# Performance work log

Hardware: AMD Instinct MI355X
Metric: run time of the kernel (lower is better)

Reference implementation:

```python
import jax, jax.numpy as jnp
import numpy as np

B, T, C = 2, 4096, 512
P, PS, CS, MB, FD = 64, 16, 5, 128, 128


def setup_inputs() -> dict:
    key = jax.random.key(0)
    ks = jax.random.split(key, 9)
    y = jax.random.normal(ks[0], (B, T, C), jnp.float32)
    # per-timestep random patch indices into the sequence axis, sorted per patch
    patches = jnp.sort(jax.random.randint(ks[1], (T, P, PS), 0, T), axis=-1).astype(jnp.int32)
    patches_proj = jax.random.randint(ks[2], (T, P), 0, T).astype(jnp.int32)
    W_BASE = jax.random.normal(ks[3], (P, PS, CS), jnp.float32) * 0.05
    W_BIAS = jax.random.normal(ks[4], (P,), jnp.float32) * 0.05
    W_proj2 = jax.random.normal(ks[5], (C, MB), jnp.float32) * (1.0 / np.sqrt(C).astype(np.float32))
    W_proj_comp = jax.random.normal(ks[6], (C, CS), jnp.float32) * (1.0 / np.sqrt(C).astype(np.float32))
    W_presoftmax1 = jax.random.normal(ks[7], (P, P), jnp.float32) * (1.0 / np.sqrt(P).astype(np.float32))
    W_FINAL = jax.random.normal(ks[8], (MB, FD), jnp.float32) * (1.0 / np.sqrt(MB).astype(np.float32))
    return {
        'y': y,
        'W_BASE': W_BASE,
        'W_BIAS': W_BIAS,
        'W_proj2': W_proj2,
        'W_proj_comp': W_proj_comp,
        'W_presoftmax1': W_presoftmax1,
        'W_FINAL': W_FINAL,
        'patches': patches,
        'patches_proj': patches_proj,
    }


def reference(y, W_BASE, W_BIAS, W_proj2, W_proj_comp, W_presoftmax1, W_FINAL, patches, patches_proj):
    # value branch: project then gather one sequence element per (t, patch)
    bm = jnp.einsum('btc,cm->btm', y, W_proj2)          # [B,T,MB]
    mbg = bm[:, patches_proj, :]                        # [B,T,P,MB]  (MBMB)
    # score branch: compress, gather PS elements per (t, patch), weighted reduce
    yc = jnp.einsum('btc,ck->btk', y, W_proj_comp)      # [B,T,CS]
    g = yc[:, patches, :]                               # [B,T,P,PS,CS]
    res = jnp.einsum('btpsc,psc->btp', g, W_BASE) + W_BIAS   # [B,T,P]
    mix = jnp.einsum('btp,pq->btq', res, W_presoftmax1)      # [B,T,P] (no softmax in source)
    out = jnp.einsum('btp,btpm->btm', mix, mbg)              # [B,T,MB]
    return jnp.einsum('btm,mf->btf', out, W_FINAL)           # [B,T,FD]
```

## Files before the change

### kernel.cpp

```cpp
#include <hip/hip_runtime.h>
#include <hip/hip_bf16.h>

#define B_ 2
#define T_ 4096
#define C_ 512
#define P_ 64
#define PS_ 16
#define CS_ 5
#define MB_ 128
#define FD_ 128

__device__ __forceinline__ float bf_lo(unsigned u) {
  return __uint_as_float(u << 16);
}
__device__ __forceinline__ float bf_hi(unsigned u) {
  return __uint_as_float(u & 0xffff0000u);
}
__device__ __forceinline__ float rdlane_f(float v, int p) {
  return __uint_as_float((unsigned)__builtin_amdgcn_readlane((int)__float_as_uint(v), p));
}

__global__ __launch_bounds__(256) void k_prep(const float* __restrict__ y,
                                              const float* __restrict__ Wc,
                                              __hip_bfloat16* __restrict__ ycp) {
  const int lane = threadIdx.x & 63;
  const int wid  = threadIdx.x >> 6;
  float wc[40];
  {
    const float4* src = (const float4*)(Wc + lane * 40);
    #pragma unroll
    for (int j = 0; j < 10; j++) {
      float4 v = src[j];
      wc[j*4+0] = v.x; wc[j*4+1] = v.y; wc[j*4+2] = v.z; wc[j*4+3] = v.w;
    }
  }
  const int row_base = (blockIdx.x * 4 + wid) * 4;
  #pragma unroll 1
  for (int r = 0; r < 4; r++) {
    const int row = row_base + r;
    const float4* yr = (const float4*)(y + (size_t)row * C_ + lane * 8);
    float4 a = yr[0], b4 = yr[1];
    float s0 = 0.f, s1 = 0.f, s2 = 0.f, s3 = 0.f, s4 = 0.f;
    float e[8] = {a.x, a.y, a.z, a.w, b4.x, b4.y, b4.z, b4.w};
    #pragma unroll
    for (int j = 0; j < 8; j++) {
      s0 = fmaf(e[j], wc[j*5+0], s0);
      s1 = fmaf(e[j], wc[j*5+1], s1);
      s2 = fmaf(e[j], wc[j*5+2], s2);
      s3 = fmaf(e[j], wc[j*5+3], s3);
      s4 = fmaf(e[j], wc[j*5+4], s4);
    }
    #pragma unroll
    for (int off = 1; off < 64; off <<= 1) {
      s0 += __shfl_xor(s0, off); s1 += __shfl_xor(s1, off);
      s2 += __shfl_xor(s2, off); s3 += __shfl_xor(s3, off);
      s4 += __shfl_xor(s4, off);
    }
    float myv = (lane == 0) ? s0 : (lane == 1) ? s1 : (lane == 2) ? s2
              : (lane == 3) ? s3 : (lane == 4) ? s4 : 0.f;
    if (lane < 8) ycp[(size_t)row * 8 + lane] = __float2bfloat16(myv);
  }
}

__global__ __launch_bounds__(512) void k_bm(const float* __restrict__ y,
                                            const float* __restrict__ W,
                                            __hip_bfloat16* __restrict__ bmb) {
  __shared__ __align__(16) float ys[32 * 64];
  const int tid = threadIdx.x;
  const int row0 = blockIdx.x * 32;
  const int tn = tid & 127;
  const int tm = tid >> 7;
  float acc[8];
  #pragma unroll
  for (int r = 0; r < 8; r++) acc[r] = 0.f;
  for (int cc = 0; cc < C_; cc += 64) {
    __syncthreads();
    {
      int r = tid >> 4, c4 = tid & 15;
      *(float4*)&ys[r*64 + c4*4] =
          *(const float4*)&y[(size_t)(row0 + r) * C_ + cc + c4*4];
    }
    __syncthreads();
    #pragma unroll
    for (int c4 = 0; c4 < 16; c4++) {
      const int c = cc + c4*4;
      const float w0 = W[(size_t)(c+0)*MB_ + tn], w1 = W[(size_t)(c+1)*MB_ + tn],
                  w2 = W[(size_t)(c+2)*MB_ + tn], w3 = W[(size_t)(c+3)*MB_ + tn];
      #pragma unroll
      for (int r = 0; r < 8; r++) {
        float4 v = *(float4*)&ys[(tm*8 + r)*64 + c4*4];
        acc[r] = fmaf(v.x, w0, fmaf(v.y, w1, fmaf(v.z, w2, fmaf(v.w, w3, acc[r]))));
      }
    }
  }
  #pragma unroll
  for (int r = 0; r < 8; r++)
    bmb[(size_t)(row0 + tm*8 + r) * MB_ + tn] = __float2bfloat16(acc[r]);
}

__global__ __launch_bounds__(256, 2) void k_mid(
    const __hip_bfloat16* __restrict__ ycp,
    const __hip_bfloat16* __restrict__ bmb,
    const float* __restrict__ WB,
    const float* __restrict__ Wbias,
    const float* __restrict__ Wps1,
    const int* __restrict__ patches,
    const int* __restrict__ pproj,
    float* __restrict__ obm)
{
  const int lane = threadIdx.x & 63;
  const int wid  = threadIdx.x >> 6;
  const int gw   = blockIdx.x * 4 + wid;

  float wb[80];
  {
    const float4* src = (const float4*)(WB + lane * 80);
    #pragma unroll
    for (int j = 0; j < 20; j++) {
      float4 v = src[j];
      wb[j*4+0] = v.x; wb[j*4+1] = v.y; wb[j*4+2] = v.z; wb[j*4+3] = v.w;
    }
  }
  const float bias = Wbias[lane];
  float wcol[64];
  #pragma unroll
  for (int p = 0; p < 64; p++) wcol[p] = Wps1[p * 64 + lane];

  #pragma unroll 1
  for (int tt = 0; tt < 2; tt++) {
    const int t = gw * 2 + tt;
    int idx[16];
    {
      const int4* psrc = (const int4*)(patches + (size_t)t * P_ * PS_ + lane * PS_);
      #pragma unroll
      for (int j = 0; j < 4; j++) {
        int4 v = psrc[j];
        idx[j*4+0] = v.x; idx[j*4+1] = v.y; idx[j*4+2] = v.z; idx[j*4+3] = v.w;
      }
    }
    const int pp = pproj[(size_t)t * P_ + lane];

    #pragma unroll 1
    for (int b = 0; b < B_; b++) {
      const __hip_bfloat16* yb = ycp + (size_t)b * T_ * 8;
      float sum = bias;
      #pragma unroll
      for (int s = 0; s < 16; s++) {
        uint4 g = *(const uint4*)(yb + (size_t)idx[s] * 8);
        sum = fmaf(bf_lo(g.x), wb[s*5+0], sum);
        sum = fmaf(bf_hi(g.x), wb[s*5+1], sum);
        sum = fmaf(bf_lo(g.y), wb[s*5+2], sum);
        sum = fmaf(bf_hi(g.y), wb[s*5+3], sum);
        sum = fmaf(bf_lo(g.z), wb[s*5+4], sum);
      }
      float mix = 0.f;
      #pragma unroll
      for (int p = 0; p < 64; p++)
        mix = fmaf(rdlane_f(sum, p), wcol[p], mix);
      const __hip_bfloat16* bb = bmb + (size_t)b * T_ * MB_;
      float ox = 0.f, oy = 0.f;
      #pragma unroll
      for (int p = 0; p < 64; p++) {
        const float mp = rdlane_f(mix, p);
        const int row = __builtin_amdgcn_readlane(pp, p);
        unsigned v = *(const unsigned*)(bb + (size_t)row * MB_ + lane * 2);
        ox = fmaf(bf_lo(v), mp, ox);
        oy = fmaf(bf_hi(v), mp, oy);
      }
      float2 o2 = make_float2(ox, oy);
      *(float2*)(obm + ((size_t)b * T_ + t) * MB_ + lane * 2) = o2;
    }
  }
}

__global__ __launch_bounds__(512) void k_final(const float* __restrict__ obm,
                                               const float* __restrict__ WF,
                                               float* __restrict__ outp) {
  __shared__ __align__(16) float os[32 * MB_];
  const int tid = threadIdx.x;
  const int row0 = blockIdx.x * 32;
  for (int j = tid; j < 32 * MB_ / 4; j += 512)
    ((float4*)os)[j] = ((const float4*)(obm + (size_t)row0 * MB_))[j];
  __syncthreads();
  const int tn = tid & 127, tm = tid >> 7;
  float acc[8];
  #pragma unroll
  for (int r = 0; r < 8; r++) acc[r] = 0.f;
  #pragma unroll
  for (int m4 = 0; m4 < MB_ / 4; m4++) {
    const int m = m4 * 4;
    const float w0 = WF[(size_t)(m+0)*FD_ + tn], w1 = WF[(size_t)(m+1)*FD_ + tn],
                w2 = WF[(size_t)(m+2)*FD_ + tn], w3 = WF[(size_t)(m+3)*FD_ + tn];
    #pragma unroll
    for (int r = 0; r < 8; r++) {
      float4 v = *(float4*)&os[(tm*8 + r)*MB_ + m];
      acc[r] = fmaf(v.x, w0, fmaf(v.y, w1, fmaf(v.z, w2, fmaf(v.w, w3, acc[r]))));
    }
  }
  #pragma unroll
  for (int r = 0; r < 8; r++)
    outp[(size_t)(row0 + tm*8 + r) * FD_ + tn] = acc[r];
}

extern "C" void kernel_launch(void* const* d_in, const int* in_sizes, int n_in,
                              void* d_out, int out_size, void* d_ws, size_t ws_size,
                              hipStream_t stream) {
  const float* y     = (const float*)d_in[0];
  const float* WB    = (const float*)d_in[1];
  const float* Wbias = (const float*)d_in[2];
  const float* Wp2   = (const float*)d_in[3];
  const float* Wpc   = (const float*)d_in[4];
  const float* Wps1  = (const float*)d_in[5];
  const float* WF    = (const float*)d_in[6];
  const int* patches = (const int*)d_in[7];
  const int* pproj   = (const int*)d_in[8];
  float* out = (float*)d_out;

  char* ws = (char*)d_ws;
  float* obm          = (float*)(ws);
  __hip_bfloat16* bmb = (__hip_bfloat16*)(ws + 4194304);
  __hip_bfloat16* ycp = (__hip_bfloat16*)(ws + 6291456);

  k_prep <<<dim3(512), dim3(256), 0, stream>>>(y, Wpc, ycp);
  k_bm   <<<dim3(256), dim3(512), 0, stream>>>(y, Wp2, bmb);
  k_mid  <<<dim3(512), dim3(256), 0, stream>>>(ycp, bmb, WB, Wbias, Wps1,
                                               patches, pproj, obm);
  k_final<<<dim3(256), dim3(512), 0, stream>>>(obm, WF, out);
}
```

Baseline: 184.0 us.

## Replace scalar FP32 projection GEMMs with bf16 MFMA GEMM kernel

Converts y and the two projection weights to bf16 (weights transposed) and replaces the scalar FMA k_bm and k_final GEMMs with a shared templated MFMA 16x16x32 bf16 GEMM that uses a swizzled LDS layout. k_mid now writes its intermediate in bf16, halving that traffic, and k_prep also emits bf16 y. The goal is to move the dense projections onto matrix cores. In exchange it adds an extra weight-conversion launch, writes a bf16 copy of y, and loses precision from bf16 inputs to the final GEMM.

Result: faster. 151.1 us (-17.9%).

```diff
diff --git a/kernel.cpp b/kernel.cpp
--- a/kernel.cpp
+++ b/kernel.cpp
@@ -10,19 +10,28 @@
 #define MB_ 128
 #define FD_ 128
 
-__device__ __forceinline__ float bf_lo(unsigned u) {
+using f32x4 = __attribute__((ext_vector_type(4))) float;
+using s16x8 = __attribute__((ext_vector_type(8))) short;
+
+static __device__ __forceinline__ float bf_lo(unsigned u) {
   return __uint_as_float(u << 16);
 }
-__device__ __forceinline__ float bf_hi(unsigned u) {
+static __device__ __forceinline__ float bf_hi(unsigned u) {
   return __uint_as_float(u & 0xffff0000u);
 }
-__device__ __forceinline__ float rdlane_f(float v, int p) {
+static __device__ __forceinline__ float rdlane_f(float v, int p) {
   return __uint_as_float((unsigned)__builtin_amdgcn_readlane((int)__float_as_uint(v), p));
 }
-
-__global__ __launch_bounds__(256) void k_prep(const float* __restrict__ y,
-                                              const float* __restrict__ Wc,
-                                              __hip_bfloat16* __restrict__ ycp) {
+static __device__ __forceinline__ ushort bf16u(float f) {
+  unsigned x = __float_as_uint(f);
+  unsigned r = (x + 0x7fffu + ((x >> 16) & 1u)) >> 16;
+  return (ushort)r;
+}
+
+__global__ __launch_bounds__(256) void k_cvt(const float* __restrict__ y,
+                                             const float* __restrict__ Wc,
+                                             ushort* __restrict__ ybf,
+                                             ushort* __restrict__ ycp) {
   const int lane = threadIdx.x & 63;
   const int wid  = threadIdx.x >> 6;
   float wc[40];
@@ -34,14 +43,18 @@
       wc[j*4+0] = v.x; wc[j*4+1] = v.y; wc[j*4+2] = v.z; wc[j*4+3] = v.w;
     }
   }
-  const int row_base = (blockIdx.x * 4 + wid) * 4;
-  #pragma unroll 1
-  for (int r = 0; r < 4; r++) {
+  const int row_base = (blockIdx.x * 4 + wid) * 8;
+  #pragma unroll 2
+  for (int r = 0; r < 8; r++) {
     const int row = row_base + r;
     const float4* yr = (const float4*)(y + (size_t)row * C_ + lane * 8);
     float4 a = yr[0], b4 = yr[1];
+    float e[8] = {a.x, a.y, a.z, a.w, b4.x, b4.y, b4.z, b4.w};
+    union { ushort us[8]; uint4 q; } pk;
+    #pragma unroll
+    for (int j = 0; j < 8; j++) pk.us[j] = bf16u(e[j]);
+    *(uint4*)(ybf + (size_t)row * C_ + lane * 8) = pk.q;
     float s0 = 0.f, s1 = 0.f, s2 = 0.f, s3 = 0.f, s4 = 0.f;
-    float e[8] = {a.x, a.y, a.z, a.w, b4.x, b4.y, b4.z, b4.w};
     #pragma unroll
     for (int j = 0; j < 8; j++) {
       s0 = fmaf(e[j], wc[j*5+0], s0);
@@ -58,55 +71,115 @@
     }
     float myv = (lane == 0) ? s0 : (lane == 1) ? s1 : (lane == 2) ? s2
               : (lane == 3) ? s3 : (lane == 4) ? s4 : 0.f;
-    if (lane < 8) ycp[(size_t)row * 8 + lane] = __float2bfloat16(myv);
-  }
-}
-
-__global__ __launch_bounds__(512) void k_bm(const float* __restrict__ y,
-                                            const float* __restrict__ W,
-                                            __hip_bfloat16* __restrict__ bmb) {
-  __shared__ __align__(16) float ys[32 * 64];
-  const int tid = threadIdx.x;
-  const int row0 = blockIdx.x * 32;
-  const int tn = tid & 127;
-  const int tm = tid >> 7;
-  float acc[8];
+    if (lane < 8) ycp[(size_t)row * 8 + lane] = bf16u(myv);
+  }
+}
+
+__global__ __launch_bounds__(256) void k_cvtW(const float* __restrict__ Wp2,
+                                              const float* __restrict__ WF,
+                                              ushort* __restrict__ Wp2T,
+                                              ushort* __restrict__ WFT) {
+  const int id = blockIdx.x * 256 + threadIdx.x;
+  if (id < C_ * MB_) {
+    const int c = id >> 7, m = id & 127;
+    Wp2T[(size_t)m * C_ + c] = bf16u(Wp2[id]);
+  }
+  const int id2 = id - C_ * MB_;
+  if (id2 >= 0 && id2 < MB_ * FD_) {
+    const int m = id2 >> 7, f = id2 & 127;
+    WFT[(size_t)f * MB_ + m] = bf16u(WF[id2]);
+  }
+}
+
+template<int KTOT, bool OUTBF>
+__global__ __launch_bounds__(256) void k_gemm(const ushort* __restrict__ A,
+                                              const ushort* __restrict__ Bt,
+                                              void* __restrict__ Cout) {
+  __shared__ __align__(16) char smem[(64 + 128) * 128];
+  const int tid  = threadIdx.x;
+  const int lane = tid & 63;
+  const int wid  = tid >> 6;
+  const int wm = wid >> 1, wn = wid & 1;
+  const int rowA0 = blockIdx.x * 64;
+
+  f32x4 acc[2][4];
   #pragma unroll
-  for (int r = 0; r < 8; r++) acc[r] = 0.f;
-  for (int cc = 0; cc < C_; cc += 64) {
+  for (int m = 0; m < 2; m++)
+    #pragma unroll
+    for (int n = 0; n < 4; n++) acc[m][n] = (f32x4){0.f, 0.f, 0.f, 0.f};
+
+  for (int step = 0; step < KTOT / 64; step++) {
+    const int kc = step * 64;
+    uint4 ra[2], rb[4];
+    #pragma unroll
+    for (int i = 0; i < 2; i++) {
+      const int slot = tid + i * 256, r = slot >> 3, sl = slot & 7;
+      ra[i] = *(const uint4*)(A + (size_t)(rowA0 + r) * KTOT + kc + sl * 8);
+    }
+    #pragma unroll
+    for (int i = 0; i < 4; i++) {
+      const int slot = tid + i * 256, r = slot >> 3, sl = slot & 7;
+      rb[i] = *(const uint4*)(Bt + (size_t)r * KTOT + kc + sl * 8);
+    }
     __syncthreads();
-    {
-      int r = tid >> 4, c4 = tid & 15;
-      *(float4*)&ys[r*64 + c4*4] =
-          *(const float4*)&y[(size_t)(row0 + r) * C_ + cc + c4*4];
+    #pragma unroll
+    for (int i = 0; i < 2; i++) {
+      const int slot = tid + i * 256, r = slot >> 3, sl = slot & 7;
+      *(uint4*)(smem + r * 128 + ((sl * 16) ^ ((r & 7) << 4))) = ra[i];
+    }
+    #pragma unroll
+    for (int i = 0; i < 4; i++) {
+      const int slot = tid + i * 256, r = slot >> 3, sl = slot & 7;
+      *(uint4*)(smem + 8192 + r * 128 + ((sl * 16) ^ ((r & 7) << 4))) = rb[i];
     }
     __syncthreads();
     #pragma unroll
-    for (int c4 = 0; c4 < 16; c4++) {
-      const int c = cc + c4*4;
-      const float w0 = W[(size_t)(c+0)*MB_ + tn], w1 = W[(size_t)(c+1)*MB_ + tn],
-                  w2 = W[(size_t)(c+2)*MB_ + tn], w3 = W[(size_t)(c+3)*MB_ + tn];
-      #pragma unroll
-      for (int r = 0; r < 8; r++) {
-        float4 v = *(float4*)&ys[(tm*8 + r)*64 + c4*4];
-        acc[r] = fmaf(v.x, w0, fmaf(v.y, w1, fmaf(v.z, w2, fmaf(v.w, w3, acc[r]))));
-      }
+    for (int kk = 0; kk < 2; kk++) {
+      const int cb = kk * 64 + (lane >> 4) * 16;
+      s16x8 a[2], b[4];
+      #pragma unroll
+      for (int m = 0; m < 2; m++) {
+        const int r = wm * 32 + m * 16 + (lane & 15);
+        a[m] = *(const s16x8*)(smem + r * 128 + (cb ^ ((r & 7) << 4)));
+      }
+      #pragma unroll
+      for (int n = 0; n < 4; n++) {
+        const int rn = wn * 64 + n * 16 + (lane & 15);
+        b[n] = *(const s16x8*)(smem + 8192 + rn * 128 + (cb ^ ((rn & 7) << 4)));
+      }
+      #pragma unroll
+      for (int m = 0; m < 2; m++)
+        #pragma unroll
+        for (int n = 0; n < 4; n++)
+          acc[m][n] = __builtin_amdgcn_mfma_f32_16x16x32_bf16(a[m], b[n], acc[m][n], 0, 0, 0);
     }
   }
   #pragma unroll
-  for (int r = 0; r < 8; r++)
-    bmb[(size_t)(row0 + tm*8 + r) * MB_ + tn] = __float2bfloat16(acc[r]);
+  for (int m = 0; m < 2; m++) {
+    #pragma unroll
+    for (int n = 0; n < 4; n++) {
+      #pragma unroll
+      for (int reg = 0; reg < 4; reg++) {
+        const int grow = rowA0 + wm * 32 + m * 16 + (lane >> 4) * 4 + reg;
+        const int gcol = wn * 64 + n * 16 + (lane & 15);
+        if (OUTBF)
+          ((ushort*)Cout)[(size_t)grow * 128 + gcol] = bf16u(acc[m][n][reg]);
+        else
+          ((float*)Cout)[(size_t)grow * 128 + gcol] = acc[m][n][reg];
+      }
+    }
+  }
 }
 
 __global__ __launch_bounds__(256, 2) void k_mid(
-    const __hip_bfloat16* __restrict__ ycp,
-    const __hip_bfloat16* __restrict__ bmb,
+    const ushort* __restrict__ ycp,
+    const ushort* __restrict__ bmb,
     const float* __restrict__ WB,
     const float* __restrict__ Wbias,
     const float* __restrict__ Wps1,
     const int* __restrict__ patches,
     const int* __restrict__ pproj,
-    float* __restrict__ obm)
+    ushort* __restrict__ obmb)
 {
   const int lane = threadIdx.x & 63;
   const int wid  = threadIdx.x >> 6;
@@ -142,7 +215,7 @@
 
     #pragma unroll 1
     for (int b = 0; b < B_; b++) {
-      const __hip_bfloat16* yb = ycp + (size_t)b * T_ * 8;
+      const ushort* yb = ycp + (size_t)b * T_ * 8;
       float sum = bias;
       #pragma unroll
       for (int s = 0; s < 16; s++) {
@@ -157,7 +230,7 @@
       #pragma unroll
       for (int p = 0; p < 64; p++)
         mix = fmaf(rdlane_f(sum, p), wcol[p], mix);
-      const __hip_bfloat16* bb = bmb + (size_t)b * T_ * MB_;
+      const ushort* bb = bmb + (size_t)b * T_ * MB_;
       float ox = 0.f, oy = 0.f;
       #pragma unroll
       for (int p = 0; p < 64; p++) {
@@ -167,39 +240,10 @@
         ox = fmaf(bf_lo(v), mp, ox);
         oy = fmaf(bf_hi(v), mp, oy);
       }
-      float2 o2 = make_float2(ox, oy);
-      *(float2*)(obm + ((size_t)b * T_ + t) * MB_ + lane * 2) = o2;
-    }
-  }
-}
-
-__global__ __launch_bounds__(512) void k_final(const float* __restrict__ obm,
-                                               const float* __restrict__ WF,
-                                               float* __restrict__ outp) {
-  __shared__ __align__(16) float os[32 * MB_];
-  const int tid = threadIdx.x;
-  const int row0 = blockIdx.x * 32;
-  for (int j = tid; j < 32 * MB_ / 4; j += 512)
-    ((float4*)os)[j] = ((const float4*)(obm + (size_t)row0 * MB_))[j];
-  __syncthreads();
-  const int tn = tid & 127, tm = tid >> 7;
-  float acc[8];
-  #pragma unroll
-  for (int r = 0; r < 8; r++) acc[r] = 0.f;
-  #pragma unroll
-  for (int m4 = 0; m4 < MB_ / 4; m4++) {
-    const int m = m4 * 4;
-    const float w0 = WF[(size_t)(m+0)*FD_ + tn], w1 = WF[(size_t)(m+1)*FD_ + tn],
-                w2 = WF[(size_t)(m+2)*FD_ + tn], w3 = WF[(size_t)(m+3)*FD_ + tn];
-    #pragma unroll
-    for (int r = 0; r < 8; r++) {
-      float4 v = *(float4*)&os[(tm*8 + r)*MB_ + m];
-      acc[r] = fmaf(v.x, w0, fmaf(v.y, w1, fmaf(v.z, w2, fmaf(v.w, w3, acc[r]))));
-    }
-  }
-  #pragma unroll
-  for (int r = 0; r < 8; r++)
-    outp[(size_t)(row0 + tm*8 + r) * FD_ + tn] = acc[r];
+      unsigned pkd = (unsigned)bf16u(ox) | ((unsigned)bf16u(oy) << 16);
+      *(unsigned*)(obmb + ((size_t)b * T_ + t) * MB_ + lane * 2) = pkd;
+    }
+  }
 }
 
 extern "C" void kernel_launch(void* const* d_in, const int* in_sizes, int n_in,
@@ -217,13 +261,17 @@
   float* out = (float*)d_out;
 
   char* ws = (char*)d_ws;
-  float* obm          = (float*)(ws);
-  __hip_bfloat16* bmb = (__hip_bfloat16*)(ws + 4194304);
-  __hip_bfloat16* ycp = (__hip_bfloat16*)(ws + 6291456);
-
-  k_prep <<<dim3(512), dim3(256), 0, stream>>>(y, Wpc, ycp);
-  k_bm   <<<dim3(256), dim3(512), 0, stream>>>(y, Wp2, bmb);
-  k_mid  <<<dim3(512), dim3(256), 0, stream>>>(ycp, bmb, WB, Wbias, Wps1,
-                                               patches, pproj, obm);
-  k_final<<<dim3(256), dim3(512), 0, stream>>>(obm, WF, out);
-}
+  ushort* ybf  = (ushort*)(ws);
+  ushort* obmb = (ushort*)(ws);
+  ushort* bmb  = (ushort*)(ws + 8388608);
+  ushort* ycp  = (ushort*)(ws + 10485760);
+  ushort* Wp2T = (ushort*)(ws + 10616832);
+  ushort* WFT  = (ushort*)(ws + 10747904);
+
+  k_cvtW<<<dim3(320), dim3(256), 0, stream>>>(Wp2, WF, Wp2T, WFT);
+  k_cvt <<<dim3(256), dim3(256), 0, stream>>>(y, Wpc, ybf, ycp);
+  k_gemm<512, true> <<<dim3(128), dim3(256), 0, stream>>>(ybf, Wp2T, (void*)bmb);
+  k_mid <<<dim3(512), dim3(256), 0, stream>>>(ycp, bmb, WB, Wbias, Wps1,
+                                              patches, pproj, obmb);
+  k_gemm<128, false><<<dim3(128), dim3(256), 0, stream>>>(obmb, WFT, (void*)out);
+}
```
